# Kernel tuning notes

Hardware: AMD Instinct MI355X
Metric: run time of the kernel (lower is better)

Reference implementation:

```python
import jax, jax.numpy as jnp
import numpy as np

# Segment geometry (from init_kwargs): modes ['u','uv','v'] -> out_v = alpha * x_u @ W_uv
U = 128
V = 128
IN_OFF = [0, 128, 256, 384]
W_OFF = [k * U * V for k in range(8)]          # [0,16384,...,114688]
OUT_OFF = [0, 128, 256, 384]
IN_STRIDE = 512
OUT_STRIDE = 512
W_STRIDE = 8 * U * V                           # 131072
# (in_seg, w_seg, out_seg, coefficient)
PATHS = [(0, 0, 0, 1.0), (1, 1, 1, 1.0), (2, 2, 2, 1.0), (3, 3, 3, 1.0),
         (0, 4, 1, 0.5), (1, 5, 2, 0.5), (2, 6, 3, 0.5), (3, 7, 0, 0.5)]
B = 32768
E = 4  # num_embeddings (experts)


def setup_inputs() -> dict:
    key = jax.random.key(0)
    k1, k2, k3 = jax.random.split(key, 3)
    tensor_in = jax.random.normal(k1, (B, IN_STRIDE), dtype=jnp.float32)
    tensor_w = jax.random.normal(k2, (E, W_STRIDE), dtype=jnp.float32)
    tensor_w_id = jax.random.randint(k3, (B,), 0, E, dtype=jnp.int32)
    return {"tensor_in": tensor_in, "tensor_w": tensor_w, "tensor_w_id": tensor_w_id}


def _batch_linear(tensor_in, tensor_w, tensor_w_id):
    """Segmented path-indexed grouped linear (cuEquivariance BatchLinear fwd).

    tensor_in: [B, IN_STRIDE]; tensor_w: [E, W_STRIDE]; tensor_w_id: [B] int in [0,E).
    For each path (i, j, k, alpha):
        out[b, OUT_OFF[k]:+V] += alpha * x[b, IN_OFF[i]:+U] @ W[w_id[b], seg j].reshape(U, V)
    """
    nb = tensor_in.shape[0]
    ne = tensor_w.shape[0]
    onehot = jax.nn.one_hot(tensor_w_id, ne, dtype=tensor_in.dtype)  # [B, E]
    out = jnp.zeros((nb, OUT_STRIDE), dtype=tensor_in.dtype)
    for (i, j, k, a) in PATHS:
        x = tensor_in[:, IN_OFF[i]:IN_OFF[i] + U]                    # [B, U]
        w_seg = tensor_w[:, W_OFF[j]:W_OFF[j] + U * V].reshape(ne, U, V)
        # masked per-expert dense GEMMs (small fixed expert count)
        y = jnp.zeros((nb, V), dtype=tensor_in.dtype)
        for e in range(ne):
            y = y + onehot[:, e:e + 1] * (x @ w_seg[e])              # [B, V]
        out = out.at[:, OUT_OFF[k]:OUT_OFF[k] + V].add(a * y)
    return out


def reference(tensor_in, tensor_w, tensor_w_id):
    return _batch_linear(tensor_in, tensor_w, tensor_w_id)
```

## Files before the change

kernel.cpp:

```cpp
#include <hip/hip_runtime.h>
#include <stdint.h>

#define U 128
#define V 128
#define IN_STRIDE 512
#define OUT_STRIDE 512
#define W_STRIDE (8 * U * V)
#define NB 32768

#define WS_WSHUF 0

typedef __bf16 bf16x8 __attribute__((ext_vector_type(8)));
typedef float f32x16 __attribute__((ext_vector_type(16)));
typedef unsigned int u32x4 __attribute__((ext_vector_type(4)));
typedef unsigned int u32x2 __attribute__((ext_vector_type(2)));

static __device__ __forceinline__ unsigned short f2bf(float f) {
    unsigned int u = __builtin_bit_cast(unsigned int, f);
    u += 0x7FFFu + ((u >> 16) & 1u);
    return (unsigned short)(u >> 16);
}

__global__ void prep_kernel(const float* __restrict__ w, unsigned short* __restrict__ wshuf) {
    int t = blockIdx.x * 256 + threadIdx.x;
    int lane = t & 63;
    int kt = (t >> 6) & 7;
    int nt = (t >> 9) & 3;
    int s  = (t >> 11) & 7;
    int e  = (t >> 14) & 3;
    int kbase = kt * 16 + ((lane >> 5) << 3);
    int n = nt * 32 + (lane & 31);
    const float* src = w + (size_t)e * W_STRIDE + (size_t)s * (U * V) + n;
    float sc = (s >= 4) ? 0.5f : 1.0f;
    __attribute__((aligned(16))) unsigned short o[8];
#pragma unroll
    for (int j = 0; j < 8; j++) o[j] = f2bf(src[(size_t)(kbase + j) * V] * sc);
    *(u32x4*)(wshuf + (size_t)t * 8) = *(const u32x4*)o;
}

__global__ __launch_bounds__(512, 4) void gemm_kernel(
        const float* __restrict__ x, const unsigned short* __restrict__ wshuf,
        const int* __restrict__ wid, float* __restrict__ out) {
    const int rowbase = blockIdx.x * 64;
    __shared__ unsigned short lds[64 * 512];

    const int t = threadIdx.x;

    {
        int r = t >> 3;
        int g = t & 7;
        const float* xr = x + (size_t)(rowbase + r) * IN_STRIDE;
        unsigned short* Lrow = lds + r * 512;
        int rs = r & 7;
#pragma unroll
        for (int i = 0; i < 16; i++) {
            int c = g * 4 + i * 32;
            float4 v = *(const float4*)(xr + c);
            __attribute__((aligned(8))) unsigned short h[4];
            h[0] = f2bf(v.x); h[1] = f2bf(v.y); h[2] = f2bf(v.z); h[3] = f2bf(v.w);
            int off = ((((c >> 3) ^ rs)) << 3) + (c & 7);
            *(u32x2*)(Lrow + off) = *(const u32x2*)h;
        }
    }

    const int w = t >> 6, lane = t & 63;
    const int kout = w >> 1, nhalf = w & 1;
    const int m0 = lane & 31;
    const int khalf3 = (lane >> 5);
    const int rowswz = m0 & 7;

    const int e0 = wid[rowbase + m0];
    const int e1 = wid[rowbase + m0 + 32];

    __syncthreads();

    unsigned int msk0[4], msk1[4];
#pragma unroll
    for (int e = 0; e < 4; e++) {
        msk0[e] = (e0 == e) ? 0xFFFFFFFFu : 0u;
        msk1[e] = (e1 == e) ? 0xFFFFFFFFu : 0u;
    }

    f32x16 acc00 = {}, acc01 = {}, acc10 = {}, acc11 = {};

    const int xbs0 = kout, xbs1 = (kout + 3) & 3;
    const int sgs0 = kout, sgs1 = xbs1 + 4;
    int xbs[2] = {xbs0, xbs1};
    int sgs[2] = {sgs0, sgs1};

    const unsigned short* Lr0 = lds + m0 * 512;
    const unsigned short* Lr1 = lds + (m0 + 32) * 512;

#pragma unroll
    for (int c = 0; c < 2; c++) {
        int colbase3 = xbs[c] * 16;
#pragma unroll
        for (int kt = 0; kt < 8; kt++) {
            int kabs3 = colbase3 + kt * 2 + khalf3;
            int packoff = ((kabs3 ^ rowswz) << 3);
            u32x4 a0u = *(const u32x4*)(Lr0 + packoff);
            u32x4 a1u = *(const u32x4*)(Lr1 + packoff);
#pragma unroll
            for (int e = 0; e < 4; e++) {
                const unsigned short* wseg =
                    wshuf + ((size_t)((e * 8 + sgs[c]) * 4 + nhalf * 2) * 8) * 512;
                bf16x8 b0 = __builtin_bit_cast(bf16x8, *(const u32x4*)(wseg + (size_t)kt * 512 + lane * 8));
                bf16x8 b1 = __builtin_bit_cast(bf16x8, *(const u32x4*)(wseg + (size_t)(8 + kt) * 512 + lane * 8));
                u32x4 mm0 = {msk0[e], msk0[e], msk0[e], msk0[e]};
                u32x4 mm1 = {msk1[e], msk1[e], msk1[e], msk1[e]};
                bf16x8 a0m = __builtin_bit_cast(bf16x8, a0u & mm0);
                bf16x8 a1m = __builtin_bit_cast(bf16x8, a1u & mm1);
                acc00 = __builtin_amdgcn_mfma_f32_32x32x16_bf16(a0m, b0, acc00, 0, 0, 0);
                acc01 = __builtin_amdgcn_mfma_f32_32x32x16_bf16(a0m, b1, acc01, 0, 0, 0);
                acc10 = __builtin_amdgcn_mfma_f32_32x32x16_bf16(a1m, b0, acc10, 0, 0, 0);
                acc11 = __builtin_amdgcn_mfma_f32_32x32x16_bf16(a1m, b1, acc11, 0, 0, 0);
            }
        }
    }

    const int colb = kout * 128 + nhalf * 64 + m0;
    const int rh = (lane >> 5) << 2;
#pragma unroll
    for (int q = 0; q < 4; q++) {
#pragma unroll
        for (int d = 0; d < 4; d++) {
            int reg = q * 4 + d;
            int rl = d + 8 * q + rh;
            float* o0 = out + (size_t)(rowbase + rl) * OUT_STRIDE + colb;
            float* o1 = out + (size_t)(rowbase + rl + 32) * OUT_STRIDE + colb;
            o0[0]  = acc00[reg];
            o0[32] = acc01[reg];
            o1[0]  = acc10[reg];
            o1[32] = acc11[reg];
        }
    }
}

extern "C" void kernel_launch(void* const* d_in, const int* in_sizes, int n_in,
                              void* d_out, int out_size, void* d_ws, size_t ws_size,
                              hipStream_t stream) {
    const float* x = (const float*)d_in[0];
    const float* w = (const float*)d_in[1];
    const int* wid = (const int*)d_in[2];
    float* out = (float*)d_out;

    unsigned short* wshuf = (unsigned short*)((char*)d_ws + WS_WSHUF);

    prep_kernel<<<256, 256, 0, stream>>>(w, wshuf);
    gemm_kernel<<<512, 512, 0, stream>>>(x, wshuf, wid, out);
}
```

Before: 135.2 us.

## Sort rows by expert and run single-expert GEMM for uniform tiles

Adds a scatter kernel that counts rows per expert with atomics and builds per-expert row lists. The GEMM kernel gathers rows in sorted order, and tiles whose 64 rows all share one expert run an unmasked single-expert loop instead of computing all four experts with masking. Outputs are scattered back through the saved row ids. This cuts MFMA work and weight loads by roughly four times for most tiles, at the cost of an extra launch, gathered row reads and scattered writes.

```diff
diff --git a/kernel.cpp b/kernel.cpp
--- a/kernel.cpp
+++ b/kernel.cpp
@@ -7,8 +7,11 @@
 #define OUT_STRIDE 512
 #define W_STRIDE (8 * U * V)
 #define NB 32768
+#define NE 4
 
 #define WS_WSHUF 0
+#define WS_CNT   1048576
+#define WS_SORT  1048640
 
 typedef __bf16 bf16x8 __attribute__((ext_vector_type(8)));
 typedef float f32x16 __attribute__((ext_vector_type(16)));
@@ -21,7 +24,9 @@
     return (unsigned short)(u >> 16);
 }
 
-__global__ void prep_kernel(const float* __restrict__ w, unsigned short* __restrict__ wshuf) {
+__global__ void prep_kernel(const float* __restrict__ w, unsigned short* __restrict__ wshuf,
+                            unsigned int* __restrict__ cnt) {
+    if (blockIdx.x == 0 && threadIdx.x < NE) cnt[threadIdx.x] = 0u;
     int t = blockIdx.x * 256 + threadIdx.x;
     int lane = t & 63;
     int kt = (t >> 6) & 7;
@@ -38,18 +43,45 @@
     *(u32x4*)(wshuf + (size_t)t * 8) = *(const u32x4*)o;
 }
 
+__global__ void scatter_kernel(const int* __restrict__ wid, unsigned int* __restrict__ cnt,
+                               int* __restrict__ sorted) {
+    __shared__ unsigned int lcnt[NE];
+    __shared__ unsigned int lbase[NE];
+    int t = threadIdx.x;
+    if (t < NE) lcnt[t] = 0u;
+    __syncthreads();
+    int i = blockIdx.x * 256 + t;
+    int e = wid[i];
+    unsigned int lpos = atomicAdd(&lcnt[e], 1u);
+    __syncthreads();
+    if (t < NE) lbase[t] = atomicAdd(&cnt[t], lcnt[t]);
+    __syncthreads();
+    sorted[e * NB + (int)(lbase[e] + lpos)] = i;
+}
+
 __global__ __launch_bounds__(512, 4) void gemm_kernel(
         const float* __restrict__ x, const unsigned short* __restrict__ wshuf,
-        const int* __restrict__ wid, float* __restrict__ out) {
+        const unsigned int* __restrict__ cnt, const int* __restrict__ sorted,
+        float* __restrict__ out) {
     const int rowbase = blockIdx.x * 64;
     __shared__ unsigned short lds[64 * 512];
+    __shared__ int rowid[64];
+
+    const unsigned int p1 = cnt[0];
+    const unsigned int p2 = p1 + cnt[1];
+    const unsigned int p3 = p2 + cnt[2];
 
     const int t = threadIdx.x;
 
     {
         int r = t >> 3;
         int g = t & 7;
-        const float* xr = x + (size_t)(rowbase + r) * IN_STRIDE;
+        unsigned int l = (unsigned int)(rowbase + r);
+        int e = (l >= p1) + (l >= p2) + (l >= p3);
+        unsigned int pe = (e == 0) ? 0u : (e == 1) ? p1 : (e == 2) ? p2 : p3;
+        int row = sorted[e * NB + (int)(l - pe)];
+        if (g == 0) rowid[r] = row;
+        const float* xr = x + (size_t)row * IN_STRIDE;
         unsigned short* Lrow = lds + r * 512;
         int rs = r & 7;
 #pragma unroll
@@ -69,51 +101,77 @@
     const int khalf3 = (lane >> 5);
     const int rowswz = m0 & 7;
 
-    const int e0 = wid[rowbase + m0];
-    const int e1 = wid[rowbase + m0 + 32];
-
-    __syncthreads();
-
-    unsigned int msk0[4], msk1[4];
-#pragma unroll
-    for (int e = 0; e < 4; e++) {
-        msk0[e] = (e0 == e) ? 0xFFFFFFFFu : 0u;
-        msk1[e] = (e1 == e) ? 0xFFFFFFFFu : 0u;
-    }
+    const unsigned int l0 = (unsigned int)(rowbase + m0);
+    const unsigned int l1 = l0 + 32u;
+    const int e0 = (l0 >= p1) + (l0 >= p2) + (l0 >= p3);
+    const int e1 = (l1 >= p1) + (l1 >= p2) + (l1 >= p3);
+    const unsigned int lh = (unsigned int)rowbase, lt = (unsigned int)(rowbase + 63);
+    const int ehead = (lh >= p1) + (lh >= p2) + (lh >= p3);
+    const int etail = (lt >= p1) + (lt >= p2) + (lt >= p3);
+
+    __syncthreads();
 
     f32x16 acc00 = {}, acc01 = {}, acc10 = {}, acc11 = {};
 
-    const int xbs0 = kout, xbs1 = (kout + 3) & 3;
-    const int sgs0 = kout, sgs1 = xbs1 + 4;
-    int xbs[2] = {xbs0, xbs1};
-    int sgs[2] = {sgs0, sgs1};
+    const int xbs1 = (kout + 3) & 3;
+    int xbs[2] = {kout, xbs1};
+    int sgs[2] = {kout, xbs1 + 4};
 
     const unsigned short* Lr0 = lds + m0 * 512;
     const unsigned short* Lr1 = lds + (m0 + 32) * 512;
 
-#pragma unroll
-    for (int c = 0; c < 2; c++) {
-        int colbase3 = xbs[c] * 16;
-#pragma unroll
-        for (int kt = 0; kt < 8; kt++) {
-            int kabs3 = colbase3 + kt * 2 + khalf3;
-            int packoff = ((kabs3 ^ rowswz) << 3);
-            u32x4 a0u = *(const u32x4*)(Lr0 + packoff);
-            u32x4 a1u = *(const u32x4*)(Lr1 + packoff);
-#pragma unroll
-            for (int e = 0; e < 4; e++) {
-                const unsigned short* wseg =
-                    wshuf + ((size_t)((e * 8 + sgs[c]) * 4 + nhalf * 2) * 8) * 512;
-                bf16x8 b0 = __builtin_bit_cast(bf16x8, *(const u32x4*)(wseg + (size_t)kt * 512 + lane * 8));
-                bf16x8 b1 = __builtin_bit_cast(bf16x8, *(const u32x4*)(wseg + (size_t)(8 + kt) * 512 + lane * 8));
-                u32x4 mm0 = {msk0[e], msk0[e], msk0[e], msk0[e]};
-                u32x4 mm1 = {msk1[e], msk1[e], msk1[e], msk1[e]};
-                bf16x8 a0m = __builtin_bit_cast(bf16x8, a0u & mm0);
-                bf16x8 a1m = __builtin_bit_cast(bf16x8, a1u & mm1);
-                acc00 = __builtin_amdgcn_mfma_f32_32x32x16_bf16(a0m, b0, acc00, 0, 0, 0);
-                acc01 = __builtin_amdgcn_mfma_f32_32x32x16_bf16(a0m, b1, acc01, 0, 0, 0);
-                acc10 = __builtin_amdgcn_mfma_f32_32x32x16_bf16(a1m, b0, acc10, 0, 0, 0);
-                acc11 = __builtin_amdgcn_mfma_f32_32x32x16_bf16(a1m, b1, acc11, 0, 0, 0);
+    if (ehead == etail) {
+        const int eu = ehead;
+#pragma unroll
+        for (int c = 0; c < 2; c++) {
+            int colbase3 = xbs[c] * 16;
+            const unsigned short* wseg =
+                wshuf + ((size_t)((eu * 8 + sgs[c]) * 4 + nhalf * 2) * 8) * 512 + (size_t)lane * 8;
+#pragma unroll
+            for (int kt = 0; kt < 8; kt++) {
+                int kabs3 = colbase3 + kt * 2 + khalf3;
+                int packoff = ((kabs3 ^ rowswz) << 3);
+                bf16x8 a0 = __builtin_bit_cast(bf16x8, *(const u32x4*)(Lr0 + packoff));
+                bf16x8 a1 = __builtin_bit_cast(bf16x8, *(const u32x4*)(Lr1 + packoff));
+                bf16x8 b0 = __builtin_bit_cast(bf16x8, *(const u32x4*)(wseg + (size_t)kt * 512));
+                bf16x8 b1 = __builtin_bit_cast(bf16x8, *(const u32x4*)(wseg + (size_t)(8 + kt) * 512));
+                acc00 = __builtin_amdgcn_mfma_f32_32x32x16_bf16(a0, b0, acc00, 0, 0, 0);
+                acc01 = __builtin_amdgcn_mfma_f32_32x32x16_bf16(a0, b1, acc01, 0, 0, 0);
+                acc10 = __builtin_amdgcn_mfma_f32_32x32x16_bf16(a1, b0, acc10, 0, 0, 0);
+                acc11 = __builtin_amdgcn_mfma_f32_32x32x16_bf16(a1, b1, acc11, 0, 0, 0);
+            }
+        }
+    } else {
+        unsigned int msk0[4], msk1[4];
+#pragma unroll
+        for (int e = 0; e < 4; e++) {
+            msk0[e] = (e0 == e) ? 0xFFFFFFFFu : 0u;
+            msk1[e] = (e1 == e) ? 0xFFFFFFFFu : 0u;
+        }
+#pragma unroll
+        for (int c = 0; c < 2; c++) {
+            int colbase3 = xbs[c] * 16;
+#pragma unroll
+            for (int kt = 0; kt < 8; kt++) {
+                int kabs3 = colbase3 + kt * 2 + khalf3;
+                int packoff = ((kabs3 ^ rowswz) << 3);
+                u32x4 a0u = *(const u32x4*)(Lr0 + packoff);
+                u32x4 a1u = *(const u32x4*)(Lr1 + packoff);
+#pragma unroll
+                for (int e = 0; e < 4; e++) {
+                    const unsigned short* wseg =
+                        wshuf + ((size_t)((e * 8 + sgs[c]) * 4 + nhalf * 2) * 8) * 512;
+                    bf16x8 b0 = __builtin_bit_cast(bf16x8, *(const u32x4*)(wseg + (size_t)kt * 512 + lane * 8));
+                    bf16x8 b1 = __builtin_bit_cast(bf16x8, *(const u32x4*)(wseg + (size_t)(8 + kt) * 512 + lane * 8));
+                    u32x4 mm0 = {msk0[e], msk0[e], msk0[e], msk0[e]};
+                    u32x4 mm1 = {msk1[e], msk1[e], msk1[e], msk1[e]};
+                    bf16x8 a0m = __builtin_bit_cast(bf16x8, a0u & mm0);
+                    bf16x8 a1m = __builtin_bit_cast(bf16x8, a1u & mm1);
+                    acc00 = __builtin_amdgcn_mfma_f32_32x32x16_bf16(a0m, b0, acc00, 0, 0, 0);
+                    acc01 = __builtin_amdgcn_mfma_f32_32x32x16_bf16(a0m, b1, acc01, 0, 0, 0);
+                    acc10 = __builtin_amdgcn_mfma_f32_32x32x16_bf16(a1m, b0, acc10, 0, 0, 0);
+                    acc11 = __builtin_amdgcn_mfma_f32_32x32x16_bf16(a1m, b1, acc11, 0, 0, 0);
+                }
             }
         }
     }
@@ -126,8 +184,8 @@
         for (int d = 0; d < 4; d++) {
             int reg = q * 4 + d;
             int rl = d + 8 * q + rh;
-            float* o0 = out + (size_t)(rowbase + rl) * OUT_STRIDE + colb;
-            float* o1 = out + (size_t)(rowbase + rl + 32) * OUT_STRIDE + colb;
+            float* o0 = out + (size_t)rowid[rl] * OUT_STRIDE + colb;
+            float* o1 = out + (size_t)rowid[rl + 32] * OUT_STRIDE + colb;
             o0[0]  = acc00[reg];
             o0[32] = acc01[reg];
             o1[0]  = acc10[reg];
@@ -145,7 +203,10 @@
     float* out = (float*)d_out;
 
     unsigned short* wshuf = (unsigned short*)((char*)d_ws + WS_WSHUF);
-
-    prep_kernel<<<256, 256, 0, stream>>>(w, wshuf);
-    gemm_kernel<<<512, 512, 0, stream>>>(x, wshuf, wid, out);
-}
+    unsigned int* cnt = (unsigned int*)((char*)d_ws + WS_CNT);
+    int* sorted = (int*)((char*)d_ws + WS_SORT);
+
+    prep_kernel<<<256, 256, 0, stream>>>(w, wshuf, cnt);
+    scatter_kernel<<<128, 256, 0, stream>>>(wid, cnt, sorted);
+    gemm_kernel<<<512, 512, 0, stream>>>(x, wshuf, cnt, sorted, out);
+}
```

Measured after the change: 134.9 us. Within noise of the previous version (-0.2%).
